# Performance work log

Measured on AMD Instinct MI355X. Metric: run time of the kernel, lower is better.

The kernel has to match this reference:

```python
import jax, jax.numpy as jnp
import numpy as np

N_STATE = 64
N_LAYERS = 3


def setup_inputs() -> dict:
    key = jax.random.key(0)
    B, L, D = 8, 8192, 64
    H = 2 * D
    ks = jax.random.split(key, 10)
    x = jax.random.normal(ks[0], (B, L, D), dtype=jnp.float32)
    W_in = jax.random.normal(ks[1], (D, H), dtype=jnp.float32) * 0.05
    b_in = jnp.zeros((H,), jnp.float32)
    # S4D parameterization: dt log-uniform in [1e-3, 1e-1], A = -0.5 + i*pi*n (S4D-Lin init)
    log_dt = jax.random.uniform(ks[2], (N_LAYERS, H), dtype=jnp.float32,
                                minval=float(np.log(1e-3)), maxval=float(np.log(1e-1)))
    log_A_real = jnp.full((N_LAYERS, H, N_STATE), float(np.log(0.5)), jnp.float32)
    A_imag = jnp.tile(jnp.pi * jnp.arange(N_STATE, dtype=jnp.float32), (N_LAYERS, H, 1))
    C_re = jax.random.normal(ks[3], (N_LAYERS, H, N_STATE), dtype=jnp.float32) * (0.5 ** 0.5)
    C_im = jax.random.normal(ks[4], (N_LAYERS, H, N_STATE), dtype=jnp.float32) * (0.5 ** 0.5)
    D_skip = jax.random.normal(ks[5], (N_LAYERS, H), dtype=jnp.float32)
    W_glu = jax.random.normal(ks[6], (N_LAYERS, 2 * H, H), dtype=jnp.float32) * 0.05
    b_glu = jnp.zeros((N_LAYERS, 2 * H), jnp.float32)
    W_out = jax.random.normal(ks[7], (H, D), dtype=jnp.float32) * 0.05
    b_out = jnp.zeros((D,), jnp.float32)
    return {"x": x, "W_in": W_in, "b_in": b_in, "log_dt": log_dt,
            "log_A_real": log_A_real, "A_imag": A_imag, "C_re": C_re, "C_im": C_im,
            "D_skip": D_skip, "W_glu": W_glu, "b_glu": b_glu,
            "W_out": W_out, "b_out": b_out}


def _s4_block(u, log_dt, log_A_real, A_imag, C_re, C_im, D_skip, W_glu, b_glu):
    # u: (B, H, L). S4D: diagonal SSM applied as a long FFT convolution.
    H, L = u.shape[1], u.shape[2]
    dt = jnp.exp(log_dt)[:, None]                       # (H,1)
    A = -jnp.exp(log_A_real) + 1j * A_imag              # (H,N), Re(A)<0 -> stable
    dtA = dt * A                                        # (H,N)
    C = (C_re + 1j * C_im) * jnp.expm1(dtA) / A         # ZOH-discretized C*B
    vand = jnp.exp(dtA[:, :, None] * jnp.arange(L, dtype=jnp.float32))  # (H,N,L)
    K = 2.0 * jnp.einsum('hn,hnl->hl', C, vand).real    # (H,L) SSM kernel
    n = 2 * L
    y = jnp.fft.irfft(jnp.fft.rfft(u, n=n) * jnp.fft.rfft(K, n=n), n=n)[..., :L]
    y = y + u * D_skip[:, None]                         # skip connection D*u
    y = jax.nn.gelu(y)
    z = jnp.einsum('bhl,gh->bgl', y, W_glu) + b_glu[None, :, None]  # pointwise H->2H
    a, g = jnp.split(z, 2, axis=1)
    return a * jax.nn.sigmoid(g)                        # GLU


def _rmsnorm(x):
    # F.normalize(x, dim=-1) * sqrt(dim)
    scale = jnp.sqrt(jnp.asarray(x.shape[-1], jnp.float32))
    nrm = jnp.linalg.norm(x, axis=-1, keepdims=True)
    return x / jnp.maximum(nrm, 1e-12) * scale


def reference(x, W_in, b_in, log_dt, log_A_real, A_imag, C_re, C_im,
              D_skip, W_glu, b_glu, W_out, b_out):
    h = x @ W_in + b_in                                 # (B,L,H)
    for i in range(N_LAYERS):
        u = h.swapaxes(-1, -2)                          # (B,H,L)
        y = _s4_block(u, log_dt[i], log_A_real[i], A_imag[i], C_re[i], C_im[i],
                      D_skip[i], W_glu[i], b_glu[i]).swapaxes(-1, -2)
        h = _rmsnorm(y + h)                             # PreNormResidual
    return h @ W_out + b_out
```

## Files before the change

### kernel.cpp

```cpp
#include <hip/hip_runtime.h>
#include <math.h>

#define BB 8
#define LL 8192
#define DD 64
#define HH 128
#define NN 64
#define NLAYER 3
#define LC 64
#define NC 128
#define LST 137
#define SIS 136

typedef _Float16 half_t;
typedef _Float16 f16x8_t __attribute__((ext_vector_type(8)));
typedef _Float16 f16x4_t __attribute__((ext_vector_type(4)));
typedef _Float16 f16x2_t __attribute__((ext_vector_type(2)));
typedef float    f32x4_t __attribute__((ext_vector_type(4)));

#define SZ_WB   ((size_t)HH*NN*2)
#define SZ_WGT  ((size_t)NLAYER*256*HH/2)
#define SZ_WOT  ((size_t)DD*HH/2)
#define SZ_WIT  ((size_t)HH*DD/2)
#define SZ_AM   ((size_t)HH*64*192/2)
#define SZ_HT   ((size_t)BB*HH*LL/2)
#define SZ_YT   ((size_t)BB*HH*LL/2)

__global__ __launch_bounds__(256) void kPrep(const float* __restrict__ logdt,
   const float* __restrict__ logA, const float* __restrict__ Aim,
   const float* __restrict__ Cre, const float* __restrict__ Cim,
   const float* __restrict__ Wglu, const float* __restrict__ Wout,
   const float* __restrict__ Win,
   float* __restrict__ wb3, float* __restrict__ wl3, half_t* __restrict__ Amat3,
   half_t* __restrict__ wgt, half_t* __restrict__ woT, half_t* __restrict__ wiT) {
  __shared__ float  ktap[4][64];
  __shared__ half_t gst[4][64][128];
  int bid = blockIdx.x;
  int t = threadIdx.x;
  if (bid < 96) {
    int layer = bid >> 5;
    int blk   = bid & 31;
    float* wb = wb3 + (size_t)layer*SZ_WB;
    float* wl = wl3 + (size_t)layer*SZ_WB;
    half_t* Amat = Amat3 + (size_t)layer*HH*64*192;
    int w = t >> 6;
    int n = t & 63;
    int h = blk*4 + w;
    float dt = expf(logdt[layer*HH + h]);
    int idx = (layer*HH + h)*NN + n;
    float ar = -expf(logA[idx]);
    float ai = Aim[idx];
    float er = expf(dt*ar);
    float wr = er*cosf(dt*ai), wi = er*sinf(dt*ai);
    float inv = 1.f/(ar*ar + ai*ai);
    float mr = wr - 1.f, mi = wi;
    float tr = (mr*ar + mi*ai)*inv;
    float ti = (mi*ar - mr*ai)*inv;
    float c0 = Cre[idx], c1 = Cim[idx];
    float cr = c0*tr - c1*ti, ci = c0*ti + c1*tr;
    wb[(h*NN+n)*2] = wr; wb[(h*NN+n)*2+1] = wi;
    float pr = 1.f, pi = 0.f;
    float qr = cr*wr - ci*wi, qi = cr*wi + ci*wr;
    for (int d = 0; d < 64; d++) {
      float kd = cr*pr - ci*pi;
      kd += __shfl_xor(kd, 1);  kd += __shfl_xor(kd, 2);  kd += __shfl_xor(kd, 4);
      kd += __shfl_xor(kd, 8);  kd += __shfl_xor(kd, 16); kd += __shfl_xor(kd, 32);
      if (n == 0) ktap[w][d] = 2.f*kd;
      f16x2_t g2 = { (half_t)(2.f*qr), (half_t)(-2.f*qi) };
      *(f16x2_t*)&gst[w][d][2*n] = g2;
      float npr = pr*wr - pi*wi, npi = pr*wi + pi*wr; pr = npr; pi = npi;
      float nqr = qr*wr - qi*wi, nqi = qr*wi + qi*wr; qr = nqr; qi = nqi;
    }
    wl[(h*NN+n)*2] = pr; wl[(h*NN+n)*2+1] = pi;
    __syncthreads();
    #pragma unroll
    for (int i = 0; i < 16; i++) {
      int idx2 = t + i*256;
      int hh = idx2 >> 10;
      int rem = idx2 & 1023;
      int l = rem >> 4, m8 = rem & 15;
      half_t* Ahh = Amat + (size_t)(blk*4 + hh)*64*192;
      *(f16x8_t*)&Ahh[(size_t)l*192 + 64 + m8*8] = *(const f16x8_t*)&gst[hh][l][m8*8];
    }
    #pragma unroll
    for (int i = 0; i < 8; i++) {
      int idx2 = t + i*256;
      int hh = idx2 >> 9;
      int rem = idx2 & 511;
      int l = rem >> 3, m8 = rem & 7;
      half_t* Ahh = Amat + (size_t)(blk*4 + hh)*64*192;
      f16x8_t v;
      #pragma unroll
      for (int j = 0; j < 8; j++) {
        int m = m8*8 + j;
        v[j] = (half_t)((m <= l) ? ktap[hh][l - m] : 0.f);
      }
      *(f16x8_t*)&Ahh[(size_t)l*192 + m8*8] = v;
    }
  } else if (bid < 144) {
    int tid = (bid - 96)*256 + t;
    const float* src = Wglu + (size_t)tid*8;
    f16x8_t v;
    #pragma unroll
    for (int i = 0; i < 8; i++) v[i] = (half_t)src[i];
    *(f16x8_t*)&wgt[(size_t)tid*8] = v;
  } else if (bid < 176) {
    int tid = (bid - 144)*256 + t;
    int d = tid >> 7, h = tid & 127;
    woT[d*HH + h] = (half_t)Wout[h*DD + d];
  } else {
    int tid = (bid - 176)*256 + t;
    int h = tid >> 6, d = tid & 63;
    wiT[h*DD + d] = (half_t)Win[d*HH + h];
  }
}

__global__ __launch_bounds__(256) void kIn(const float* __restrict__ x,
      const half_t* __restrict__ wiT, const float* __restrict__ bin,
      half_t* __restrict__ hT) {
  __shared__ half_t xs[64*72];
  __shared__ half_t zs[128*72];
  size_t row0 = (size_t)blockIdx.x * 64;
  int t = threadIdx.x;
  #pragma unroll
  for (int i = 0; i < 4; i++) {
    int idx = t + i*256;
    int r = idx >> 4, c4 = idx & 15;
    float4 v = *(const float4*)&x[(row0 + r)*DD + c4*4];
    f16x4_t o = { (half_t)v.x, (half_t)v.y, (half_t)v.z, (half_t)v.w };
    *(f16x4_t*)&xs[r*72 + c4*4] = o;
  }
  __syncthreads();
  int wid = t >> 6, lane = t & 63;
  int lr = lane & 15, lq = lane >> 4, lk = lq*8;
  f32x4_t acc[4][2];
  #pragma unroll
  for (int mr = 0; mr < 4; mr++)
    #pragma unroll
    for (int nc = 0; nc < 2; nc++) {
      float bv = bin[(wid*2 + nc)*16 + lr];
      acc[mr][nc] = (f32x4_t){bv, bv, bv, bv};
    }
  #pragma unroll
  for (int ks = 0; ks < 2; ks++) {
    int k = ks*32 + lk;
    f16x8_t af[4], bf[2];
    #pragma unroll
    for (int mr = 0; mr < 4; mr++) af[mr] = *(const f16x8_t*)&xs[(mr*16 + lr)*72 + k];
    #pragma unroll
    for (int nc = 0; nc < 2; nc++)
      bf[nc] = *(const f16x8_t*)&wiT[(size_t)((wid*2 + nc)*16 + lr)*DD + k];
    #pragma unroll
    for (int mr = 0; mr < 4; mr++)
      #pragma unroll
      for (int nc = 0; nc < 2; nc++)
        acc[mr][nc] = __builtin_amdgcn_mfma_f32_16x16x32_f16(af[mr], bf[nc], acc[mr][nc], 0, 0, 0);
  }
  #pragma unroll
  for (int mr = 0; mr < 4; mr++)
    #pragma unroll
    for (int nc = 0; nc < 2; nc++) {
      int h = (wid*2 + nc)*16 + lr;
      f16x4_t v = { (half_t)acc[mr][nc][0], (half_t)acc[mr][nc][1],
                    (half_t)acc[mr][nc][2], (half_t)acc[mr][nc][3] };
      *(f16x4_t*)&zs[h*72 + mr*16 + lq*4] = v;
    }
  __syncthreads();
  size_t bb = row0 >> 13;
  int l0 = (int)(row0 & 8191);
  int h = t >> 1, hf = t & 1;
  half_t* dst = hT + ((size_t)bb*HH + h)*LL + l0 + hf*32;
  #pragma unroll
  for (int j = 0; j < 4; j++)
    *(f16x8_t*)&dst[j*8] = *(const f16x8_t*)&zs[h*72 + hf*32 + j*8];
}

__global__ __launch_bounds__(512) void kG(const half_t* __restrict__ hT,
      const float* __restrict__ wb, const float* __restrict__ wl,
      const half_t* __restrict__ Amat, half_t* __restrict__ yT) {
  __shared__ half_t va[128*72];
  __shared__ half_t ub[128*72];
  __shared__ half_t spad[128*LST];
  __shared__ float  segT[8*128];
  int t = threadIdx.x;
  int h = blockIdx.x >> 3, b = blockIdx.x & 7;
  {
    int n = t >> 3, q8 = t & 7;
    float wr = wb[(h*NN+n)*2], wi = wb[(h*NN+n)*2+1];
    float ar = wr, ai = wi;
    #pragma unroll
    for (int i = 0; i < 3; i++) { float nr = ar*ar - ai*ai, ni = 2.f*ar*ai; ar = nr; ai = ni; }
    float pr = 1.f, pi = 0.f;
    for (int e = 0; e < 7 - q8; e++) { float nr = pr*ar - pi*ai, ni = pr*ai + pi*ar; pr = nr; pi = ni; }
    int k0 = (7 - q8)*8;
    for (int i = 0; i < 8; i++) {
      int m = 63 - (k0 + i);
      va[(2*n)*72 + m]   = (half_t)pr;
      va[(2*n+1)*72 + m] = (half_t)pi;
      float nr = pr*wr - pi*wi, ni = pr*wi + pi*wr; pr = nr; pi = ni;
    }
  }
  {
    const half_t* src = hT + ((size_t)b*HH + h)*LL;
    #pragma unroll
    for (int i = 0; i < 2; i++) {
      int idx = t + i*512;
      int row = idx >> 3, off = (idx & 7)*8;
      *(f16x8_t*)&ub[row*72 + off] = *(const f16x8_t*)&src[row*64 + off];
    }
  }
  __syncthreads();
  int wid = t >> 6, lane = t & 63;
  int lr = lane & 15, lq = lane >> 4, lk = lq*8;
  {
    int wr_ = wid & 1, wc = wid >> 1;
    f32x4_t acc[4][2];
    #pragma unroll
    for (int mr = 0; mr < 4; mr++) { acc[mr][0] = (f32x4_t){0.f,0.f,0.f,0.f}; acc[mr][1] = (f32x4_t){0.f,0.f,0.f,0.f}; }
    #pragma unroll
    for (int ks = 0; ks < 2; ks++) {
      int k = ks*32 + lk;
      f16x8_t af[4], bf[2];
      #pragma unroll
      for (int mr = 0; mr < 4; mr++) af[mr] = *(const f16x8_t*)&va[(wr_*64 + mr*16 + lr)*72 + k];
      #pragma unroll
      for (int nc = 0; nc < 2; nc++) bf[nc] = *(const f16x8_t*)&ub[(wc*32 + nc*16 + lr)*72 + k];
      #pragma unroll
      for (int mr = 0; mr < 4; mr++)
        #pragma unroll
        for (int nc = 0; nc < 2; nc++)
          acc[mr][nc] = __builtin_amdgcn_mfma_f32_16x16x32_f16(af[mr], bf[nc], acc[mr][nc], 0, 0, 0);
    }
    #pragma unroll
    for (int mr = 0; mr < 4; mr++)
      #pragma unroll
      for (int nc = 0; nc < 2; nc++)
        #pragma unroll
        for (int r = 0; r < 4; r++)
          spad[(wr_*64 + mr*16 + lq*4 + r)*LST + (wc*32 + nc*16 + lr)] = (half_t)acc[mr][nc][r];
  }
  __syncthreads();
  {
    int n = t & 63, seg = t >> 6;
    int c0 = seg*16;
    float w64r = wl[(h*NN+n)*2], w64i = wl[(h*NN+n)*2+1];
    float pregr[16], pregi[16];
    float cr = 0.f, ci = 0.f;
    #pragma unroll
    for (int i = 0; i < 16; i++) {
      int c = c0 + i;
      float lre = (float)spad[(2*n)*LST + c];
      float lim = (float)spad[(2*n+1)*LST + c];
      pregr[i] = cr; pregi[i] = ci;
      float nr = fmaf(w64r, cr, fmaf(-w64i, ci, lre));
      float ni = fmaf(w64i, cr, fmaf(w64r, ci, lim));
      cr = nr; ci = ni;
    }
    segT[seg*128 + 2*n] = cr; segT[seg*128 + 2*n+1] = ci;
    __syncthreads();
    float ar = w64r, ai = w64i;
    #pragma unroll
    for (int i = 0; i < 4; i++) { float nr = ar*ar - ai*ai, ni = 2.f*ar*ai; ar = nr; ai = ni; }
    float br = 0.f, bi = 0.f;
    for (int k = 0; k < seg; k++) {
      float tr_ = segT[k*128 + 2*n], ti_ = segT[k*128 + 2*n+1];
      float nr = fmaf(ar, br, fmaf(-ai, bi, tr_));
      float ni = fmaf(ai, br, fmaf(ar, bi, ti_));
      br = nr; bi = ni;
    }
    float wpr = 1.f, wpi = 0.f;
    #pragma unroll
    for (int i = 0; i < 16; i++) {
      int c = c0 + i;
      float sr = pregr[i] + wpr*br - wpi*bi;
      float si = pregi[i] + wpr*bi + wpi*br;
      f16x2_t v = { (half_t)sr, (half_t)si };
      *(f16x2_t*)&spad[c*SIS + 2*n] = v;
      float nr = wpr*w64r - wpi*w64i, ni = wpr*w64i + wpi*w64r;
      wpr = nr; wpi = ni;
    }
  }
  __syncthreads();
  {
    const half_t* Ag = Amat + (size_t)h*64*192;
    f32x4_t acc[4];
    #pragma unroll
    for (int mr = 0; mr < 4; mr++) acc[mr] = (f32x4_t){0.f,0.f,0.f,0.f};
    int c = wid*16 + lr;
    #pragma unroll
    for (int ks = 0; ks < 6; ks++) {
      int k = ks*32 + lk;
      f16x8_t af[4];
      #pragma unroll
      for (int mr = 0; mr < 4; mr++) af[mr] = *(const f16x8_t*)&Ag[(size_t)(mr*16 + lr)*192 + k];
      f16x8_t bf = (ks < 2) ? *(const f16x8_t*)&ub[c*72 + k]
                            : *(const f16x8_t*)&spad[c*SIS + (k - 64)];
      #pragma unroll
      for (int mr = 0; mr < 4; mr++)
        acc[mr] = __builtin_amdgcn_mfma_f32_16x16x32_f16(af[mr], bf, acc[mr], 0, 0, 0);
    }
    #pragma unroll
    for (int mr = 0; mr < 4; mr++) {
      int l0 = mr*16 + lq*4;
      f16x4_t v = { (half_t)acc[mr][0], (half_t)acc[mr][1],
                    (half_t)acc[mr][2], (half_t)acc[mr][3] };
      *(f16x4_t*)&va[c*72 + l0] = v;
    }
  }
  __syncthreads();
  {
    half_t* yp = yT + ((size_t)b*HH + h)*LL;
    int c = t >> 2, q = t & 3;
    const half_t* src = &va[c*72 + q*16];
    f16x8_t v0 = *(const f16x8_t*)src;
    f16x8_t v1 = *(const f16x8_t*)(src + 8);
    *(f16x8_t*)&yp[c*64 + q*16]     = v0;
    *(f16x8_t*)&yp[c*64 + q*16 + 8] = v1;
  }
}

__global__ __launch_bounds__(256) void kD(const half_t* __restrict__ yT,
     const half_t* __restrict__ hTin, const float* __restrict__ dskip,
     const half_t* __restrict__ wgt, const float* __restrict__ bglu,
     half_t* __restrict__ hT, const half_t* __restrict__ woT,
     const float* __restrict__ bout, float* __restrict__ out, int last) {
  __shared__ half_t ylds[64][136];
  __shared__ half_t ulds[64][136];
  __shared__ float  rpart[4][64];
  size_t row0 = (size_t)blockIdx.x * 64;
  int b  = (int)(row0 >> 13);
  int l0 = (int)(row0 & 8191);
  int t = threadIdx.x;
  int h  = t >> 1, hf = t & 1;
  int lbase = hf*32;
  const half_t* yb  = yT   + ((size_t)b*HH + h)*LL + l0 + lbase;
  const half_t* ubp = hTin + ((size_t)b*HH + h)*LL + l0 + lbase;
  float d = dskip[h];
  #pragma unroll
  for (int j = 0; j < 4; j++) {
    f16x8_t yv = *(const f16x8_t*)&yb[j*8];
    f16x8_t uv = *(const f16x8_t*)&ubp[j*8];
    #pragma unroll
    for (int i = 0; i < 8; i++) {
      float v = fmaf((float)uv[i], d, (float)yv[i]);
      float arg2 = 1.5957691216057308f*(v + 0.044715f*v*v*v);
      arg2 = fminf(fmaxf(arg2, -30.f), 30.f);
      float e = __expf(-arg2);
      float o = v * __builtin_amdgcn_rcpf(1.f + e);
      ylds[lbase + j*8 + i][h] = (half_t)o;
      ulds[lbase + j*8 + i][h] = uv[i];
    }
  }
  __syncthreads();
  {
    int w = t >> 6, lane = t & 63;
    int lr = lane & 15, lq = lane >> 4;
    f16x8_t af[4][4];
    #pragma unroll
    for (int mt = 0; mt < 4; mt++)
      #pragma unroll
      for (int ks = 0; ks < 4; ks++)
        af[mt][ks] = *(const f16x8_t*)&ylds[mt*16 + lr][ks*32 + lq*8];
    __syncthreads();
    int ntl[4] = { 2*w, 2*w+1, 2*w+8, 2*w+9 };
    f32x4_t acc[4][4];
    #pragma unroll
    for (int mt = 0; mt < 4; mt++)
      #pragma unroll
      for (int p = 0; p < 4; p++) acc[mt][p] = (f32x4_t){0.f,0.f,0.f,0.f};
    #pragma unroll
    for (int p = 0; p < 4; p++) {
      int nt = ntl[p];
      #pragma unroll
      for (int ks = 0; ks < 4; ks++) {
        f16x8_t bf = *(const f16x8_t*)&wgt[(size_t)(nt*16 + lr)*HH + ks*32 + lq*8];
        #pragma unroll
        for (int mt = 0; mt < 4; mt++)
          acc[mt][p] = __builtin_amdgcn_mfma_f32_16x16x32_f16(af[mt][ks], bf, acc[mt][p], 0, 0, 0);
      }
    }
    float sp[4][4];
    #pragma unroll
    for (int mt = 0; mt < 4; mt++)
      #pragma unroll
      for (int r = 0; r < 4; r++) sp[mt][r] = 0.f;
    #pragma unroll
    for (int p = 0; p < 2; p++) {
      int col = 32*w + p*16 + lr;
      float ba = bglu[col], bg = bglu[col + 128];
      #pragma unroll
      for (int mt = 0; mt < 4; mt++)
        #pragma unroll
        for (int r = 0; r < 4; r++) {
          int row = mt*16 + lq*4 + r;
          float a = acc[mt][p][r]   + ba;
          float g = acc[mt][p+2][r] + bg;
          float s = __builtin_amdgcn_rcpf(1.f + __expf(-g));
          float z = a*s + (float)ulds[row][col];
          ylds[row][col] = (half_t)z;
          sp[mt][r] = fmaf(z, z, sp[mt][r]);
        }
    }
    #pragma unroll
    for (int m = 1; m < 16; m <<= 1)
      #pragma unroll
      for (int mt = 0; mt < 4; mt++)
        #pragma unroll
        for (int r = 0; r < 4; r++) sp[mt][r] += __shfl_xor(sp[mt][r], m);
    if (lr == 0) {
      #pragma unroll
      for (int mt = 0; mt < 4; mt++)
        #pragma unroll
        for (int r = 0; r < 4; r++) rpart[w][mt*16 + lq*4 + r] = sp[mt][r];
    }
  }
  __syncthreads();
  f16x8_t o[4];
  #pragma unroll
  for (int j = 0; j < 4; j++)
    #pragma unroll
    for (int i = 0; i < 8; i++) {
      int row = lbase + j*8 + i;
      float rn = rpart[0][row] + rpart[1][row] + rpart[2][row] + rpart[3][row];
      float sc = 11.313708498984761f * __builtin_amdgcn_rsqf(fmaxf(rn, 1e-24f));
      o[j][i] = (half_t)((float)ylds[row][h]*sc);
    }
  if (!last) {
    half_t* hb = hT + ((size_t)b*HH + h)*LL + l0 + lbase;
    #pragma unroll
    for (int j = 0; j < 4; j++) *(f16x8_t*)&hb[j*8] = o[j];
  } else {
    #pragma unroll
    for (int j = 0; j < 4; j++)
      #pragma unroll
      for (int i = 0; i < 8; i++) ulds[lbase + j*8 + i][h] = o[j][i];
    __syncthreads();
    int w = t >> 6, lane = t & 63;
    int lr = lane & 15, lq = lane >> 4;
    int dd = w*16 + lr;
    f32x4_t oacc[4];
    float bv = bout[dd];
    #pragma unroll
    for (int mt = 0; mt < 4; mt++) oacc[mt] = (f32x4_t){bv, bv, bv, bv};
    #pragma unroll
    for (int ks = 0; ks < 4; ks++) {
      int k = ks*32 + lq*8;
      f16x8_t bf = *(const f16x8_t*)&woT[(size_t)dd*HH + k];
      #pragma unroll
      for (int mt = 0; mt < 4; mt++) {
        f16x8_t af2 = *(const f16x8_t*)&ulds[mt*16 + lr][k];
        oacc[mt] = __builtin_amdgcn_mfma_f32_16x16x32_f16(af2, bf, oacc[mt], 0, 0, 0);
      }
    }
    #pragma unroll
    for (int mt = 0; mt < 4; mt++)
      #pragma unroll
      for (int r = 0; r < 4; r++)
        out[(row0 + mt*16 + lq*4 + r)*DD + dd] = oacc[mt][r];
  }
}

extern "C" void kernel_launch(void* const* d_in, const int* in_sizes, int n_in,
                              void* d_out, int out_size, void* d_ws, size_t ws_size,
                              hipStream_t stream) {
  const float* x     = (const float*)d_in[0];
  const float* Win   = (const float*)d_in[1];
  const float* bin   = (const float*)d_in[2];
  const float* logdt = (const float*)d_in[3];
  const float* logA  = (const float*)d_in[4];
  const float* Aim   = (const float*)d_in[5];
  const float* Cre   = (const float*)d_in[6];
  const float* Cim   = (const float*)d_in[7];
  const float* Dsk   = (const float*)d_in[8];
  const float* Wglu  = (const float*)d_in[9];
  const float* bglu  = (const float*)d_in[10];
  const float* Wout  = (const float*)d_in[11];
  const float* bout  = (const float*)d_in[12];
  float* out = (float*)d_out;

  float* ws   = (float*)d_ws;
  float* wb3  = ws;
  float* wl3  = wb3 + 3*SZ_WB;
  float* wgtF = wl3 + 3*SZ_WB;
  float* woTF = wgtF + SZ_WGT;
  float* wiTF = woTF + SZ_WOT;
  float* amF  = wiTF + SZ_WIT;
  float* htF  = amF + 3*SZ_AM;
  float* ytF  = htF + SZ_HT;
  half_t* wgt    = (half_t*)wgtF;
  half_t* woT    = (half_t*)woTF;
  half_t* wiT    = (half_t*)wiTF;
  half_t* Amat3  = (half_t*)amF;
  half_t* hT     = (half_t*)htF;
  half_t* yT     = (half_t*)ytF;

  kPrep<<<dim3(208), dim3(256), 0, stream>>>(logdt, logA, Aim, Cre, Cim,
                                             Wglu, Wout, Win,
                                             wb3, wl3, Amat3, wgt, woT, wiT);
  kIn<<<dim3(1024), dim3(256), 0, stream>>>(x, wiT, bin, hT);

  for (int layer = 0; layer < NLAYER; ++layer) {
    const float* wb = wb3 + (size_t)layer*SZ_WB;
    const float* wl = wl3 + (size_t)layer*SZ_WB;
    const half_t* Amat = Amat3 + (size_t)layer*HH*64*192;
    kG<<<dim3(1024), dim3(512), 0, stream>>>(hT, wb, wl, Amat, yT);
    kD<<<dim3(1024), dim3(256), 0, stream>>>(yT, hT, Dsk + layer*HH,
                       wgt + (size_t)layer*256*HH,
                       bglu + layer*2*HH, hT, woT, bout, out,
                       (layer == NLAYER-1) ? 1 : 0);
  }
}
```

Before: 225.5 us.

## Double kD block size to 512 threads and redistribute GLU and output GEMM work

The GLU/RMSnorm kernel kD now runs 512 threads per block instead of 256. Each thread handles 16 sequence positions per channel instead of 32, and each of the 8 waves computes one 16-column tile pair (value and gate) of the GLU GEMM. The final output projection is split across 8 waves by row halves. This lowers per-thread register use and adds in-flight parallelism for the memory-bound elementwise part, at the cost of more reduction partials and more redundant weight loads per block.

```diff
diff --git a/kernel.cpp b/kernel.cpp
--- a/kernel.cpp
+++ b/kernel.cpp
@@ -319,25 +319,25 @@
   }
 }
 
-__global__ __launch_bounds__(256) void kD(const half_t* __restrict__ yT,
+__global__ __launch_bounds__(512) void kD(const half_t* __restrict__ yT,
      const half_t* __restrict__ hTin, const float* __restrict__ dskip,
      const half_t* __restrict__ wgt, const float* __restrict__ bglu,
      half_t* __restrict__ hT, const half_t* __restrict__ woT,
      const float* __restrict__ bout, float* __restrict__ out, int last) {
   __shared__ half_t ylds[64][136];
   __shared__ half_t ulds[64][136];
-  __shared__ float  rpart[4][64];
+  __shared__ float  rpart[8][64];
   size_t row0 = (size_t)blockIdx.x * 64;
   int b  = (int)(row0 >> 13);
   int l0 = (int)(row0 & 8191);
   int t = threadIdx.x;
-  int h  = t >> 1, hf = t & 1;
-  int lbase = hf*32;
+  int h = t >> 2, q = t & 3;
+  int lbase = q*16;
   const half_t* yb  = yT   + ((size_t)b*HH + h)*LL + l0 + lbase;
   const half_t* ubp = hTin + ((size_t)b*HH + h)*LL + l0 + lbase;
   float d = dskip[h];
   #pragma unroll
-  for (int j = 0; j < 4; j++) {
+  for (int j = 0; j < 2; j++) {
     f16x8_t yv = *(const f16x8_t*)&yb[j*8];
     f16x8_t uv = *(const f16x8_t*)&ubp[j*8];
     #pragma unroll
@@ -355,52 +355,39 @@
   {
     int w = t >> 6, lane = t & 63;
     int lr = lane & 15, lq = lane >> 4;
-    f16x8_t af[4][4];
+    f32x4_t acc[4][2];
+    #pragma unroll
+    for (int mt = 0; mt < 4; mt++) { acc[mt][0] = (f32x4_t){0.f,0.f,0.f,0.f}; acc[mt][1] = (f32x4_t){0.f,0.f,0.f,0.f}; }
+    #pragma unroll
+    for (int ks = 0; ks < 4; ks++) {
+      int k = ks*32 + lq*8;
+      f16x8_t af[4];
+      #pragma unroll
+      for (int mt = 0; mt < 4; mt++) af[mt] = *(const f16x8_t*)&ylds[mt*16 + lr][k];
+      f16x8_t bfa = *(const f16x8_t*)&wgt[(size_t)(w*16 + lr)*HH + k];
+      f16x8_t bfg = *(const f16x8_t*)&wgt[(size_t)((w + 8)*16 + lr)*HH + k];
+      #pragma unroll
+      for (int mt = 0; mt < 4; mt++) {
+        acc[mt][0] = __builtin_amdgcn_mfma_f32_16x16x32_f16(af[mt], bfa, acc[mt][0], 0, 0, 0);
+        acc[mt][1] = __builtin_amdgcn_mfma_f32_16x16x32_f16(af[mt], bfg, acc[mt][1], 0, 0, 0);
+      }
+    }
+    __syncthreads();
+    int col = w*16 + lr;
+    float ba = bglu[col], bg = bglu[col + 128];
+    float sp[4][4];
     #pragma unroll
     for (int mt = 0; mt < 4; mt++)
       #pragma unroll
-      for (int ks = 0; ks < 4; ks++)
-        af[mt][ks] = *(const f16x8_t*)&ylds[mt*16 + lr][ks*32 + lq*8];
-    __syncthreads();
-    int ntl[4] = { 2*w, 2*w+1, 2*w+8, 2*w+9 };
-    f32x4_t acc[4][4];
-    #pragma unroll
-    for (int mt = 0; mt < 4; mt++)
-      #pragma unroll
-      for (int p = 0; p < 4; p++) acc[mt][p] = (f32x4_t){0.f,0.f,0.f,0.f};
-    #pragma unroll
-    for (int p = 0; p < 4; p++) {
-      int nt = ntl[p];
-      #pragma unroll
-      for (int ks = 0; ks < 4; ks++) {
-        f16x8_t bf = *(const f16x8_t*)&wgt[(size_t)(nt*16 + lr)*HH + ks*32 + lq*8];
-        #pragma unroll
-        for (int mt = 0; mt < 4; mt++)
-          acc[mt][p] = __builtin_amdgcn_mfma_f32_16x16x32_f16(af[mt][ks], bf, acc[mt][p], 0, 0, 0);
+      for (int r = 0; r < 4; r++) {
+        int row = mt*16 + lq*4 + r;
+        float a = acc[mt][0][r] + ba;
+        float g = acc[mt][1][r] + bg;
+        float s = __builtin_amdgcn_rcpf(1.f + __expf(-g));
+        float z = a*s + (float)ulds[row][col];
+        ylds[row][col] = (half_t)z;
+        sp[mt][r] = z*z;
       }
-    }
-    float sp[4][4];
-    #pragma unroll
-    for (int mt = 0; mt < 4; mt++)
-      #pragma unroll
-      for (int r = 0; r < 4; r++) sp[mt][r] = 0.f;
-    #pragma unroll
-    for (int p = 0; p < 2; p++) {
-      int col = 32*w + p*16 + lr;
-      float ba = bglu[col], bg = bglu[col + 128];
-      #pragma unroll
-      for (int mt = 0; mt < 4; mt++)
-        #pragma unroll
-        for (int r = 0; r < 4; r++) {
-          int row = mt*16 + lq*4 + r;
-          float a = acc[mt][p][r]   + ba;
-          float g = acc[mt][p+2][r] + bg;
-          float s = __builtin_amdgcn_rcpf(1.f + __expf(-g));
-          float z = a*s + (float)ulds[row][col];
-          ylds[row][col] = (half_t)z;
-          sp[mt][r] = fmaf(z, z, sp[mt][r]);
-        }
-    }
     #pragma unroll
     for (int m = 1; m < 16; m <<= 1)
       #pragma unroll
@@ -415,48 +402,56 @@
     }
   }
   __syncthreads();
-  f16x8_t o[4];
-  #pragma unroll
-  for (int j = 0; j < 4; j++)
-    #pragma unroll
-    for (int i = 0; i < 8; i++) {
-      int row = lbase + j*8 + i;
-      float rn = rpart[0][row] + rpart[1][row] + rpart[2][row] + rpart[3][row];
-      float sc = 11.313708498984761f * __builtin_amdgcn_rsqf(fmaxf(rn, 1e-24f));
-      o[j][i] = (half_t)((float)ylds[row][h]*sc);
-    }
+  f16x8_t o0, o1;
+  #pragma unroll
+  for (int i = 0; i < 8; i++) {
+    int row = lbase + i;
+    float rn = rpart[0][row] + rpart[1][row] + rpart[2][row] + rpart[3][row]
+             + rpart[4][row] + rpart[5][row] + rpart[6][row] + rpart[7][row];
+    float sc = 11.313708498984761f * __builtin_amdgcn_rsqf(fmaxf(rn, 1e-24f));
+    o0[i] = (half_t)((float)ylds[row][h]*sc);
+  }
+  #pragma unroll
+  for (int i = 0; i < 8; i++) {
+    int row = lbase + 8 + i;
+    float rn = rpart[0][row] + rpart[1][row] + rpart[2][row] + rpart[3][row]
+             + rpart[4][row] + rpart[5][row] + rpart[6][row] + rpart[7][row];
+    float sc = 11.313708498984761f * __builtin_amdgcn_rsqf(fmaxf(rn, 1e-24f));
+    o1[i] = (half_t)((float)ylds[row][h]*sc);
+  }
   if (!last) {
     half_t* hb = hT + ((size_t)b*HH + h)*LL + l0 + lbase;
-    #pragma unroll
-    for (int j = 0; j < 4; j++) *(f16x8_t*)&hb[j*8] = o[j];
+    *(f16x8_t*)hb = o0;
+    *(f16x8_t*)(hb + 8) = o1;
   } else {
     #pragma unroll
-    for (int j = 0; j < 4; j++)
-      #pragma unroll
-      for (int i = 0; i < 8; i++) ulds[lbase + j*8 + i][h] = o[j][i];
+    for (int i = 0; i < 8; i++) ulds[lbase + i][h]     = o0[i];
+    #pragma unroll
+    for (int i = 0; i < 8; i++) ulds[lbase + 8 + i][h] = o1[i];
     __syncthreads();
     int w = t >> 6, lane = t & 63;
     int lr = lane & 15, lq = lane >> 4;
-    int dd = w*16 + lr;
-    f32x4_t oacc[4];
+    int dd = (w & 3)*16 + lr;
+    int mth = (w >> 2)*2;
+    f32x4_t oacc[2];
     float bv = bout[dd];
-    #pragma unroll
-    for (int mt = 0; mt < 4; mt++) oacc[mt] = (f32x4_t){bv, bv, bv, bv};
+    oacc[0] = (f32x4_t){bv, bv, bv, bv};
+    oacc[1] = (f32x4_t){bv, bv, bv, bv};
     #pragma unroll
     for (int ks = 0; ks < 4; ks++) {
       int k = ks*32 + lq*8;
       f16x8_t bf = *(const f16x8_t*)&woT[(size_t)dd*HH + k];
       #pragma unroll
-      for (int mt = 0; mt < 4; mt++) {
-        f16x8_t af2 = *(const f16x8_t*)&ulds[mt*16 + lr][k];
-        oacc[mt] = __builtin_amdgcn_mfma_f32_16x16x32_f16(af2, bf, oacc[mt], 0, 0, 0);
+      for (int j = 0; j < 2; j++) {
+        f16x8_t af2 = *(const f16x8_t*)&ulds[(mth + j)*16 + lr][k];
+        oacc[j] = __builtin_amdgcn_mfma_f32_16x16x32_f16(af2, bf, oacc[j], 0, 0, 0);
       }
     }
     #pragma unroll
-    for (int mt = 0; mt < 4; mt++)
+    for (int j = 0; j < 2; j++)
       #pragma unroll
       for (int r = 0; r < 4; r++)
-        out[(row0 + mt*16 + lq*4 + r)*DD + dd] = oacc[mt][r];
+        out[(row0 + (mth + j)*16 + lq*4 + r)*DD + dd] = oacc[j][r];
   }
 }
 
@@ -504,7 +499,7 @@
     const float* wl = wl3 + (size_t)layer*SZ_WB;
     const half_t* Amat = Amat3 + (size_t)layer*HH*64*192;
     kG<<<dim3(1024), dim3(512), 0, stream>>>(hT, wb, wl, Amat, yT);
-    kD<<<dim3(1024), dim3(256), 0, stream>>>(yT, hT, Dsk + layer*HH,
+    kD<<<dim3(1024), dim3(512), 0, stream>>>(yT, hT, Dsk + layer*HH,
                        wgt + (size_t)layer*256*HH,
                        bglu + layer*2*HH, hT, woT, bout, out,
                        (layer == NLAYER-1) ? 1 : 0);
```

After: 223.0 us (median of 2 runs). About the same (-1.1%).
